# Optimization experiments

Measured on AMD Instinct MI355X. Metric: run time of the kernel, lower is better.

Reference implementation:

```python
import jax, jax.numpy as jnp
import numpy as np

N = 50000
E = 1000000
D_IN = 128
D_HID = 128
D_EMB = 128
D_DEG = 32
NEG_SLOPE = 0.2


def _add_self_loops(src, dst, n):
    loop = jnp.arange(n, dtype=src.dtype)
    return jnp.concatenate([src, loop]), jnp.concatenate([dst, loop])


def gat_conv(x, src, dst, W, a_src, a_dst, b, n):
    """PyG GATConv, heads=1, add_self_loops=True. src/dst already include self loops."""
    h = x @ W                                   # [n, d_out]
    hs = h[src]                                 # [e, d_out] gather (message sources)
    e = jax.nn.leaky_relu(hs @ a_src + h[dst] @ a_dst, NEG_SLOPE)  # [e]
    m = jax.ops.segment_max(e, dst, num_segments=n)
    e = jnp.exp(e - m[dst])
    denom = jax.ops.segment_sum(e, dst, num_segments=n)
    alpha = e / (denom[dst] + 1e-16)
    out = jax.ops.segment_sum(alpha[:, None] * hs, dst, num_segments=n)
    return out + b


def setup_inputs() -> dict:
    key = jax.random.key(0)
    ks = jax.random.split(key, 24)
    p = lambda k, shape: (jax.random.normal(k, shape, dtype=jnp.float32) * 0.05)
    inp = {
        "x_o": jax.random.normal(ks[0], (N, D_IN), dtype=jnp.float32),
        "degree_o": jax.random.normal(ks[1], (N, D_DEG), dtype=jnp.float32),
        "edge_index_o": jax.random.randint(ks[2], (2, E), 0, N, dtype=jnp.int32),
        "edge_index_s": jax.random.randint(ks[3], (2, E), 0, N, dtype=jnp.int32),
        # GAT layer params: o1, o2, s1, s2
        "W_o1": p(ks[4], (D_IN, D_HID)), "a_src_o1": p(ks[5], (D_HID,)), "a_dst_o1": p(ks[6], (D_HID,)), "b_o1": jnp.zeros((D_HID,), jnp.float32),
        "W_o2": p(ks[7], (D_HID, D_EMB)), "a_src_o2": p(ks[8], (D_EMB,)), "a_dst_o2": p(ks[9], (D_EMB,)), "b_o2": jnp.zeros((D_EMB,), jnp.float32),
        "W_s1": p(ks[10], (D_IN, D_HID)), "a_src_s1": p(ks[11], (D_HID,)), "a_dst_s1": p(ks[12], (D_HID,)), "b_s1": jnp.zeros((D_HID,), jnp.float32),
        "W_s2": p(ks[13], (D_HID, D_EMB)), "a_src_s2": p(ks[14], (D_EMB,)), "a_dst_s2": p(ks[15], (D_EMB,)), "b_s2": jnp.zeros((D_EMB,), jnp.float32),
        "W_pred": p(ks[16], (2 * D_EMB + D_DEG, 2)), "b_pred": jnp.zeros((2,), jnp.float32),
    }
    return inp


def reference(x_o, degree_o,
              W_o1, a_src_o1, a_dst_o1, b_o1,
              W_o2, a_src_o2, a_dst_o2, b_o2,
              W_s1, a_src_s1, a_dst_s1, b_s1,
              W_s2, a_src_s2, a_dst_s2, b_s2,
              W_pred, b_pred,
              edge_index_o, edge_index_s):
    n = x_o.shape[0]
    src_o, dst_o = _add_self_loops(edge_index_o[0], edge_index_o[1], n)
    src_s, dst_s = _add_self_loops(edge_index_s[0], edge_index_s[1], n)

    # branch o (original graph); dropout is identity in eval mode
    x1_o = jax.nn.relu(gat_conv(x_o, src_o, dst_o, W_o1, a_src_o1, a_dst_o1, b_o1, n))
    x2_o = gat_conv(x1_o, src_o, dst_o, W_o2, a_src_o2, a_dst_o2, b_o2, n)
    # branch s (second graph)
    x1_s = jax.nn.relu(gat_conv(x_o, src_s, dst_s, W_s1, a_src_s1, a_dst_s1, b_s1, n))
    x2_s = gat_conv(x1_s, src_s, dst_s, W_s2, a_src_s2, a_dst_s2, b_s2, n)

    x2_os = jnp.concatenate([x2_o, x2_s, degree_o], axis=1)   # [n, 2*emb+deg]
    attn = jax.nn.softmax(x2_os @ W_pred + b_pred, axis=1)    # [n, 2]
    pred = attn[:, :1] * x2_o + attn[:, 1:] * x2_s            # [n, emb]
    return pred
```

## Files before the change

kernel.cpp:

```cpp
#include <hip/hip_runtime.h>
#include <hip/hip_fp16.h>
#include <math.h>


#define LRELU(v) ((v) > 0.f ? (v) : 0.2f * (v))

#define BSHIFT 7
#define BSIZE  128
#define MAXB   512
#define CHUNK  4096
#define EPT    16
#define MAXE   4352
#define CAPI   (MAXE + BSIZE)
#define WTSZ   17408

typedef _Float16 half8 __attribute__((ext_vector_type(8)));
typedef float f32x4 __attribute__((ext_vector_type(4)));


__global__ __launch_bounds__(256) void k_bin_scatter(
    const int* __restrict__ src_o, const int* __restrict__ dst_o,
    const int* __restrict__ src_s, const int* __restrict__ dst_s,
    int* bcur_o, int* bcur_s, int* ebin_o, int* ebin_s, int E)
{
    __shared__ int cnt[MAXB];
    __shared__ int gb[MAXB];
    int t = threadIdx.x;
    int base = blockIdx.x * CHUNK;

    for (int g = 0; g < 2; g++) {
        const int* srcp = g ? src_s : src_o;
        const int* dstp = g ? dst_s : dst_o;
        int* bcur = g ? bcur_s : bcur_o;
        int* ebin = g ? ebin_s : ebin_o;
        for (int i = t; i < MAXB; i += 256) cnt[i] = 0;
        __syncthreads();
        int pk[EPT], bk[EPT], rk[EPT];
        #pragma unroll
        for (int j = 0; j < EPT; j++) {
            int e = base + j * 256 + t;
            bk[j] = -1; pk[j] = 0; rk[j] = 0;
            if (e < E) {
                int d = dstp[e];
                int s = srcp[e];
                int bb = d >> BSHIFT;
                bk[j] = bb;
                pk[j] = ((d & (BSIZE - 1)) << 16) | s;
                rk[j] = atomicAdd(&cnt[bb], 1);
            }
        }
        __syncthreads();
        for (int i = t; i < MAXB; i += 256) {
            int c = cnt[i];
            gb[i] = c ? atomicAdd(&bcur[i], c) : 0;
        }
        __syncthreads();
        #pragma unroll
        for (int j = 0; j < EPT; j++) {
            if (bk[j] >= 0) {
                int p = gb[bk[j]] + rk[j];
                if (p < (bk[j] + 1) * MAXE) ebin[p] = pk[j];
            }
        }
        __syncthreads();
    }
}

__global__ __launch_bounds__(256) void k_sort(
    const int* __restrict__ ebin_o, const int* __restrict__ bcur_o,
    int* __restrict__ off_o, int* __restrict__ dend_o, unsigned short* __restrict__ idx_o,
    const int* __restrict__ ebin_s, const int* __restrict__ bcur_s,
    int* __restrict__ off_s, int* __restrict__ dend_s, unsigned short* __restrict__ idx_s,
    int N)
{
    const int* ebin = blockIdx.y ? ebin_s : ebin_o;
    const int* bcur = blockIdx.y ? bcur_s : bcur_o;
    int* off  = blockIdx.y ? off_s  : off_o;
    int* dend = blockIdx.y ? dend_s : dend_o;
    unsigned short* idx = blockIdx.y ? idx_s : idx_o;

    __shared__ int pack[MAXE];
    __shared__ int sorted[MAXE + BSIZE];
    __shared__ int cnt4[4][BSIZE + 1];
    __shared__ int s2[BSIZE + 1];
    __shared__ int noff[BSIZE + 1];

    int b = blockIdx.x;
    int t = threadIdx.x;
    int wave = t >> 6;
    int node0 = b << BSHIFT;
    int nloc = min(BSIZE, N - node0);
    int ebeg = b * MAXE;
    int ne = min(bcur[b] - ebeg, MAXE);
    int ib = b * CAPI;

    for (int i = t; i < ne; i += 256) pack[i] = ebin[ebeg + i];
    for (int i = t; i < 4 * (BSIZE + 1); i += 256) ((int*)cnt4)[i] = 0;
    __syncthreads();
    for (int i = t; i < ne; i += 256) atomicAdd(&cnt4[wave][pack[i] >> 16], 1);
    __syncthreads();
    int c0 = 0, c1 = 0, c2 = 0, c3 = 0, selfc = 0;
    if (t < BSIZE + 1) {
        c0 = cnt4[0][t]; c1 = cnt4[1][t]; c2 = cnt4[2][t]; c3 = cnt4[3][t];
        selfc = (t < nloc) ? 1 : 0;
        s2[t] = c0 + c1 + c2 + c3 + selfc;
    }
    __syncthreads();
    for (int d = 1; d <= BSIZE; d <<= 1) {
        int v = (t < BSIZE + 1 && t >= d) ? s2[t - d] : 0;
        __syncthreads();
        if (t < BSIZE + 1) s2[t] += v;
        __syncthreads();
    }
    if (t < BSIZE + 1) noff[t] = s2[t] - (c0 + c1 + c2 + c3 + selfc);
    __syncthreads();
    if (t < nloc) {
        int base0 = noff[t] + 1;
        cnt4[0][t] = base0;
        cnt4[1][t] = base0 + c0;
        cnt4[2][t] = base0 + c0 + c1;
        cnt4[3][t] = base0 + c0 + c1 + c2;
        sorted[noff[t]] = node0 + t;
        off[node0 + t]  = ib + noff[t];
        dend[node0 + t] = ib + s2[t];
    }
    __syncthreads();
    for (int i = t; i < ne; i += 256) {
        int p = atomicAdd(&cnt4[wave][pack[i] >> 16], 1);
        sorted[p] = pack[i] & 0xffff;
    }
    __syncthreads();
    int tot = ne + nloc;
    for (int i = t; i < tot; i += 256) idx[ib + i] = (unsigned short)sorted[i];
}


__global__ __launch_bounds__(256) void k_prepw(
    const float* __restrict__ W0, const float* __restrict__ W1,
    const float* __restrict__ W2, const float* __restrict__ W3,
    _Float16* __restrict__ WtG, int* bcur_o, int* bcur_s, int nbuck)
{
    int i = blockIdx.x * 256 + threadIdx.x;
    if (i < nbuck) { bcur_o[i] = i * MAXE; bcur_s[i] = i * MAXE; }
    int w = i >> 14;
    int rem = i & 16383;
    int nn = rem >> 7;
    int k = rem & 127;
    const float* W = (w == 0) ? W0 : (w == 1) ? W1 : (w == 2) ? W2 : W3;
    WtG[w * WTSZ + nn * 136 + k] = (_Float16)W[k * 128 + nn];
}


__device__ __forceinline__ void sd_epilogue(
    const f32x4* acc, const float* a_src, const float* a_dst,
    float* Svec, float* Dvec, int m0, int wave, int lane, int m, int q, int n)
{
    float sp[4] = {0.f, 0.f, 0.f, 0.f};
    float dp[4] = {0.f, 0.f, 0.f, 0.f};
    #pragma unroll
    for (int nt = 0; nt < 8; nt++) {
        float asv = a_src[nt * 16 + m];
        float adv = a_dst[nt * 16 + m];
        #pragma unroll
        for (int r = 0; r < 4; r++) {
            sp[r] = fmaf(acc[nt][r], asv, sp[r]);
            dp[r] = fmaf(acc[nt][r], adv, dp[r]);
        }
    }
    #pragma unroll
    for (int msk = 1; msk < 16; msk <<= 1) {
        #pragma unroll
        for (int r = 0; r < 4; r++) {
            sp[r] += __shfl_xor(sp[r], msk);
            dp[r] += __shfl_xor(dp[r], msk);
        }
    }
    if (m == 0) {
        #pragma unroll
        for (int r = 0; r < 4; r++) {
            int row = m0 + wave * 16 + q * 4 + r;
            if (row < n) { Svec[row] = sp[r]; Dvec[row] = dp[r]; }
        }
    }
}

__device__ __forceinline__ void d_to_lds(
    _Float16* As, const f32x4* acc, int wave, int m, int q)
{
    #pragma unroll
    for (int nt = 0; nt < 8; nt++) {
        #pragma unroll
        for (int r = 0; r < 4; r++) {
            As[(wave * 16 + q * 4 + r) * 136 + nt * 16 + m] = (_Float16)acc[nt][r];
        }
    }
}

__device__ __forceinline__ void lds_to_h(
    const _Float16* As, __half* H, int m0, int tid, int n)
{
    for (int i = tid; i < 1024; i += 256) {
        int r = i >> 4;
        int c8 = (i & 15) << 3;
        int row = m0 + r;
        if (row < n)
            *(uint4*)&H[(size_t)row * 128 + c8] = *(const uint4*)&As[r * 136 + c8];
    }
}


__global__ __launch_bounds__(256, 4) void k_gemm1(
    const float* __restrict__ X,
    const _Float16* __restrict__ WtO, const _Float16* __restrict__ WtS,
    const float* __restrict__ asO, const float* __restrict__ adO,
    const float* __restrict__ asS, const float* __restrict__ adS,
    __half* __restrict__ HO, __half* __restrict__ HS,
    float* __restrict__ SO, float* __restrict__ DO,
    float* __restrict__ SS, float* __restrict__ DS, int n)
{
    __shared__ _Float16 As[64 * 136];
    __shared__ _Float16 Wt[128 * 136];
    int tid = threadIdx.x;
    int m0 = blockIdx.x * 64;

    for (int i = tid; i < WTSZ / 8; i += 256)
        ((uint4*)Wt)[i] = ((const uint4*)WtO)[i];
    for (int i = tid; i < 64 * 32; i += 256) {
        int r = i >> 5;
        int c4 = (i & 31) << 2;
        int row = m0 + r; if (row >= n) row = n - 1;
        float4 v = *(const float4*)&X[(size_t)row * 128 + c4];
        _Float16* p = &As[r * 136 + c4];
        p[0] = (_Float16)v.x; p[1] = (_Float16)v.y;
        p[2] = (_Float16)v.z; p[3] = (_Float16)v.w;
    }
    __syncthreads();

    int wave = tid >> 6;
    int lane = tid & 63;
    int m = lane & 15;
    int q = lane >> 4;
    int arow = wave * 16 + m;

    f32x4 accO[8], accS[8];
    #pragma unroll
    for (int nt = 0; nt < 8; nt++) accO[nt] = (f32x4){0.f, 0.f, 0.f, 0.f};
    #pragma unroll
    for (int k0 = 0; k0 < 128; k0 += 32) {
        half8 a = *(half8*)&As[arow * 136 + k0 + q * 8];
        #pragma unroll
        for (int nt = 0; nt < 8; nt++) {
            half8 b = *(half8*)&Wt[(nt * 16 + m) * 136 + k0 + q * 8];
            accO[nt] = __builtin_amdgcn_mfma_f32_16x16x32_f16(a, b, accO[nt], 0, 0, 0);
        }
    }
    sd_epilogue(accO, asO, adO, SO, DO, m0, wave, lane, m, q, n);
    __syncthreads();
    for (int i = tid; i < WTSZ / 8; i += 256)
        ((uint4*)Wt)[i] = ((const uint4*)WtS)[i];
    __syncthreads();
    #pragma unroll
    for (int nt = 0; nt < 8; nt++) accS[nt] = (f32x4){0.f, 0.f, 0.f, 0.f};
    #pragma unroll
    for (int k0 = 0; k0 < 128; k0 += 32) {
        half8 a = *(half8*)&As[arow * 136 + k0 + q * 8];
        #pragma unroll
        for (int nt = 0; nt < 8; nt++) {
            half8 b = *(half8*)&Wt[(nt * 16 + m) * 136 + k0 + q * 8];
            accS[nt] = __builtin_amdgcn_mfma_f32_16x16x32_f16(a, b, accS[nt], 0, 0, 0);
        }
    }
    sd_epilogue(accS, asS, adS, SS, DS, m0, wave, lane, m, q, n);

    __syncthreads();
    d_to_lds(As, accO, wave, m, q);
    __syncthreads();
    lds_to_h(As, HO, m0, tid, n);
    __syncthreads();
    d_to_lds(As, accS, wave, m, q);
    __syncthreads();
    lds_to_h(As, HS, m0, tid, n);
}


__global__ __launch_bounds__(256) void k_gemm2(
    const __half* __restrict__ X0, const __half* __restrict__ X1,
    const _Float16* __restrict__ WtA, const _Float16* __restrict__ WtB,
    const float* __restrict__ as0, const float* __restrict__ ad0,
    const float* __restrict__ as1, const float* __restrict__ ad1,
    __half* __restrict__ H0, __half* __restrict__ H1,
    float* __restrict__ S0, float* __restrict__ D0,
    float* __restrict__ S1, float* __restrict__ D1,
    int n)
{
    int br = blockIdx.y;
    const __half* X = br ? X1 : X0;
    const _Float16* WtGp = br ? WtB : WtA;
    const float* a_src = br ? as1 : as0;
    const float* a_dst = br ? ad1 : ad0;
    __half* H = br ? H1 : H0;
    float* Svec = br ? S1 : S0;
    float* Dvec = br ? D1 : D0;

    __shared__ _Float16 As[64 * 136];
    __shared__ _Float16 Wt[128 * 136];
    int tid = threadIdx.x;
    int m0 = blockIdx.x * 64;

    for (int i = tid; i < WTSZ / 8; i += 256)
        ((uint4*)Wt)[i] = ((const uint4*)WtGp)[i];
    for (int i = tid; i < 64 * 16; i += 256) {
        int r = i >> 4;
        int c8 = (i & 15) << 3;
        int row = m0 + r; if (row >= n) row = n - 1;
        *(uint4*)&As[r * 136 + c8] = *(const uint4*)&X[(size_t)row * 128 + c8];
    }
    __syncthreads();

    int wave = tid >> 6;
    int lane = tid & 63;
    int m = lane & 15;
    int q = lane >> 4;
    int arow = wave * 16 + m;

    f32x4 acc[8];
    #pragma unroll
    for (int nt = 0; nt < 8; nt++) acc[nt] = (f32x4){0.f, 0.f, 0.f, 0.f};
    #pragma unroll
    for (int k0 = 0; k0 < 128; k0 += 32) {
        half8 a = *(half8*)&As[arow * 136 + k0 + q * 8];
        #pragma unroll
        for (int nt = 0; nt < 8; nt++) {
            half8 b = *(half8*)&Wt[(nt * 16 + m) * 136 + k0 + q * 8];
            acc[nt] = __builtin_amdgcn_mfma_f32_16x16x32_f16(a, b, acc[nt], 0, 0, 0);
        }
    }
    sd_epilogue(acc, a_src, a_dst, Svec, Dvec, m0, wave, lane, m, q, n);
    __syncthreads();
    d_to_lds(As, acc, wave, m, q);
    __syncthreads();
    lds_to_h(As, H, m0, tid, n);
}


__device__ __forceinline__ void agg_core(
    const __half* __restrict__ H, const float* __restrict__ Svec, float dn,
    const unsigned short* __restrict__ idx, int beg, int end,
    int lane, int q, int subl, float* acc, float& denom)
{
    #pragma unroll
    for (int j = 0; j < 8; j++) acc[j] = 0.f;
    denom = 0.f;
    for (int base = beg; base < end; base += 64) {
        int cnt = min(64, end - base);
        float w = 0.f;
        int s = 0;
        if (lane < cnt) {
            s = idx[base + lane];
            w = __expf(LRELU(Svec[s] + dn));
        }
        denom += w;
        int cnt16 = (cnt + 15) & ~15;
        for (int kk = 0; kk < cnt16; kk += 16) {
            int k0 = kk + q;
            float w0 = __shfl(w, k0);
            float w1 = __shfl(w, k0 + 4);
            float w2 = __shfl(w, k0 + 8);
            float w3 = __shfl(w, k0 + 12);
            int s0 = __shfl(s, k0);
            int s1 = __shfl(s, k0 + 4);
            int s2 = __shfl(s, k0 + 8);
            int s3 = __shfl(s, k0 + 12);
            uint4 u0 = ((const uint4*)(H + (size_t)s0 * 128))[subl];
            uint4 u1 = ((const uint4*)(H + (size_t)s1 * 128))[subl];
            uint4 u2 = ((const uint4*)(H + (size_t)s2 * 128))[subl];
            uint4 u3 = ((const uint4*)(H + (size_t)s3 * 128))[subl];
            const _Float16* p;
            p = (const _Float16*)&u0;
            #pragma unroll
            for (int j = 0; j < 8; j++) acc[j] = fmaf((float)p[j], w0, acc[j]);
            p = (const _Float16*)&u1;
            #pragma unroll
            for (int j = 0; j < 8; j++) acc[j] = fmaf((float)p[j], w1, acc[j]);
            p = (const _Float16*)&u2;
            #pragma unroll
            for (int j = 0; j < 8; j++) acc[j] = fmaf((float)p[j], w2, acc[j]);
            p = (const _Float16*)&u3;
            #pragma unroll
            for (int j = 0; j < 8; j++) acc[j] = fmaf((float)p[j], w3, acc[j]);
        }
    }
    #pragma unroll
    for (int j = 0; j < 8; j++) {
        acc[j] += __shfl_xor(acc[j], 16);
        acc[j] += __shfl_xor(acc[j], 32);
    }
    #pragma unroll
    for (int o = 32; o; o >>= 1) denom += __shfl_xor(denom, o);
}


__global__ __launch_bounds__(256) void k_agg1(
    const __half* __restrict__ H0, const __half* __restrict__ H1,
    const float* __restrict__ S0, const float* __restrict__ D0,
    const float* __restrict__ S1, const float* __restrict__ D1,
    const int* __restrict__ off0, const int* __restrict__ dend0,
    const unsigned short* __restrict__ idx0,
    const int* __restrict__ off1, const int* __restrict__ dend1,
    const unsigned short* __restrict__ idx1,
    const float* __restrict__ b0, const float* __restrict__ b1,
    __half* __restrict__ out0, __half* __restrict__ out1,
    int n)
{
    int br = blockIdx.y;
    const __half* H = br ? H1 : H0;
    const float* Svec = br ? S1 : S0;
    const float* Dvec = br ? D1 : D0;
    const int* off  = br ? off1  : off0;
    const int* dend = br ? dend1 : dend0;
    const unsigned short* idx = br ? idx1 : idx0;
    const float* bias = br ? b1 : b0;
    __half* out = br ? out1 : out0;

    int wave = threadIdx.x >> 6;
    int lane = threadIdx.x & 63;
    int node = blockIdx.x * 4 + wave;
    if (node >= n) return;

    int q = lane >> 4;
    int subl = lane & 15;
    float acc[8], denom;
    agg_core(H, Svec, Dvec[node], idx, off[node], dend[node],
             lane, q, subl, acc, denom);

    if (q == 0) {
        float inv = 1.f / (denom + 1e-16f);
        int cb = subl << 3;
        half8 hv;
        #pragma unroll
        for (int j = 0; j < 8; j++) {
            float v = fmaxf(acc[j] * inv + bias[cb + j], 0.f);
            hv[j] = (_Float16)v;
        }
        *(half8*)&out[(size_t)node * 128 + cb] = hv;
    }
}


__global__ __launch_bounds__(256) void k_agg_pred(
    const __half* __restrict__ H0, const __half* __restrict__ H1,
    const float* __restrict__ S0, const float* __restrict__ D0,
    const float* __restrict__ S1, const float* __restrict__ D1,
    const int* __restrict__ off0, const int* __restrict__ dend0,
    const unsigned short* __restrict__ idx0,
    const int* __restrict__ off1, const int* __restrict__ dend1,
    const unsigned short* __restrict__ idx1,
    const float* __restrict__ b0, const float* __restrict__ b1,
    const float* __restrict__ deg,
    const float* __restrict__ Wp, const float* __restrict__ bp,
    float* __restrict__ out, int n)
{
    int wave = threadIdx.x >> 6;
    int lane = threadIdx.x & 63;
    int node = blockIdx.x * 4 + wave;
    if (node >= n) return;

    int q = lane >> 4;
    int subl = lane & 15;
    int cb = subl << 3;

    float acc[8], denom;
    float vo[8], vs[8];

    agg_core(H0, S0, D0[node], idx0, off0[node], dend0[node],
             lane, q, subl, acc, denom);
    {
        float inv = 1.f / (denom + 1e-16f);
        #pragma unroll
        for (int j = 0; j < 8; j++) vo[j] = acc[j] * inv + b0[cb + j];
    }
    agg_core(H1, S1, D1[node], idx1, off1[node], dend1[node],
             lane, q, subl, acc, denom);
    {
        float inv = 1.f / (denom + 1e-16f);
        #pragma unroll
        for (int j = 0; j < 8; j++) vs[j] = acc[j] * inv + b1[cb + j];
    }

    if (q == 0) {
        float z0 = 0.f, z1 = 0.f;
        #pragma unroll
        for (int j = 0; j < 8; j++) {
            int c = cb + j;
            z0 = fmaf(vo[j], Wp[c * 2],     z0);
            z1 = fmaf(vo[j], Wp[c * 2 + 1], z1);
            z0 = fmaf(vs[j], Wp[(128 + c) * 2],     z0);
            z1 = fmaf(vs[j], Wp[(128 + c) * 2 + 1], z1);
        }
        float2 dv = *(const float2*)&deg[(size_t)node * 32 + 2 * subl];
        z0 = fmaf(dv.x, Wp[(256 + 2 * subl) * 2],     z0);
        z1 = fmaf(dv.x, Wp[(256 + 2 * subl) * 2 + 1], z1);
        z0 = fmaf(dv.y, Wp[(257 + 2 * subl) * 2],     z0);
        z1 = fmaf(dv.y, Wp[(257 + 2 * subl) * 2 + 1], z1);
        #pragma unroll
        for (int msk = 1; msk < 16; msk <<= 1) {
            z0 += __shfl_xor(z0, msk);
            z1 += __shfl_xor(z1, msk);
        }
        z0 += bp[0];
        z1 += bp[1];
        float mz = fmaxf(z0, z1);
        float e0 = __expf(z0 - mz);
        float e1 = __expf(z1 - mz);
        float a0 = e0 / (e0 + e1);
        float a1 = 1.f - a0;
        float4 r0, r1;
        r0.x = a0 * vo[0] + a1 * vs[0];
        r0.y = a0 * vo[1] + a1 * vs[1];
        r0.z = a0 * vo[2] + a1 * vs[2];
        r0.w = a0 * vo[3] + a1 * vs[3];
        r1.x = a0 * vo[4] + a1 * vs[4];
        r1.y = a0 * vo[5] + a1 * vs[5];
        r1.z = a0 * vo[6] + a1 * vs[6];
        r1.w = a0 * vo[7] + a1 * vs[7];
        *(float4*)&out[(size_t)node * 128 + cb] = r0;
        *(float4*)&out[(size_t)node * 128 + cb + 4] = r1;
    }
}


extern "C" void kernel_launch(void* const* d_in, const int* in_sizes, int n_in,
                              void* d_out, int out_size, void* d_ws, size_t ws_size,
                              hipStream_t stream) {
    const float* x_o    = (const float*)d_in[0];
    const float* degree = (const float*)d_in[1];
    const int*   ei_o   = (const int*)d_in[2];
    const int*   ei_s   = (const int*)d_in[3];
    const float* W_o1 = (const float*)d_in[4];
    const float* asr_o1 = (const float*)d_in[5];
    const float* ads_o1 = (const float*)d_in[6];
    const float* b_o1 = (const float*)d_in[7];
    const float* W_o2 = (const float*)d_in[8];
    const float* asr_o2 = (const float*)d_in[9];
    const float* ads_o2 = (const float*)d_in[10];
    const float* b_o2 = (const float*)d_in[11];
    const float* W_s1 = (const float*)d_in[12];
    const float* asr_s1 = (const float*)d_in[13];
    const float* ads_s1 = (const float*)d_in[14];
    const float* b_s1 = (const float*)d_in[15];
    const float* W_s2 = (const float*)d_in[16];
    const float* asr_s2 = (const float*)d_in[17];
    const float* ads_s2 = (const float*)d_in[18];
    const float* b_s2 = (const float*)d_in[19];
    const float* W_pred = (const float*)d_in[20];
    const float* b_pred = (const float*)d_in[21];
    float* out = (float*)d_out;

    const int N = in_sizes[0] / 128;
    const int E = in_sizes[2] / 2;
    const int NBUCK = (N + BSIZE - 1) >> BSHIFT;

    char* ws = (char*)d_ws;
    size_t o = 0;
    auto alloc = [&](size_t bytes) -> char* {
        char* p = ws + o;
        o += (bytes + 255) & ~(size_t)255;
        return p;
    };
    int* bcur_o = (int*)alloc((size_t)NBUCK * 4);
    int* bcur_s = (int*)alloc((size_t)NBUCK * 4);
    int* off_o  = (int*)alloc((size_t)N * 4);
    int* dend_o = (int*)alloc((size_t)N * 4);
    int* off_s  = (int*)alloc((size_t)N * 4);
    int* dend_s = (int*)alloc((size_t)N * 4);
    unsigned short* idx_o = (unsigned short*)alloc((size_t)NBUCK * CAPI * 2);
    unsigned short* idx_s = (unsigned short*)alloc((size_t)NBUCK * CAPI * 2);
    _Float16* WtG = (_Float16*)alloc((size_t)4 * WTSZ * 2);
    float* Sv_o = (float*)alloc((size_t)N * 4);
    float* Dv_o = (float*)alloc((size_t)N * 4);
    float* Sv_s = (float*)alloc((size_t)N * 4);
    float* Dv_s = (float*)alloc((size_t)N * 4);
    __half* h_o   = (__half*)alloc((size_t)N * 128 * 2);
    __half* h_s   = (__half*)alloc((size_t)N * 128 * 2);
    __half* x1h_o = (__half*)alloc((size_t)N * 128 * 2);
    __half* x1h_s = (__half*)alloc((size_t)N * 128 * 2);
    (void)ws_size;

    int* ebin_o = (int*)h_o;
    int* ebin_s = (int*)h_s;

    dim3 blk(256);
    int gBin  = (E + CHUNK - 1) / CHUNK;
    int gGemm = (N + 63) / 64;
    int gNode = (N + 3) / 4;

    k_prepw<<<256, blk, 0, stream>>>(W_o1, W_o2, W_s1, W_s2, WtG,
                                     bcur_o, bcur_s, NBUCK);
    k_bin_scatter<<<gBin, blk, 0, stream>>>(ei_o, ei_o + E, ei_s, ei_s + E,
                                            bcur_o, bcur_s, ebin_o, ebin_s, E);
    dim3 gSort(NBUCK, 2);
    k_sort<<<gSort, blk, 0, stream>>>(ebin_o, bcur_o, off_o, dend_o, idx_o,
                                      ebin_s, bcur_s, off_s, dend_s, idx_s, N);

    k_gemm1<<<gGemm, blk, 0, stream>>>(
        x_o, WtG, WtG + 2 * WTSZ,
        asr_o1, ads_o1, asr_s1, ads_s1,
        h_o, h_s, Sv_o, Dv_o, Sv_s, Dv_s, N);
    dim3 gA(gNode, 2);
    k_agg1<<<gA, blk, 0, stream>>>(
        h_o, h_s, Sv_o, Dv_o, Sv_s, Dv_s,
        off_o, dend_o, idx_o, off_s, dend_s, idx_s,
        b_o1, b_s1, x1h_o, x1h_s, N);
    dim3 gG(gGemm, 2);
    k_gemm2<<<gG, blk, 0, stream>>>(
        x1h_o, x1h_s, WtG + WTSZ, WtG + 3 * WTSZ,
        asr_o2, ads_o2, asr_s2, ads_s2,
        h_o, h_s, Sv_o, Dv_o, Sv_s, Dv_s, N);
    k_agg_pred<<<gNode, blk, 0, stream>>>(
        h_o, h_s, Sv_o, Dv_o, Sv_s, Dv_s,
        off_o, dend_o, idx_o, off_s, dend_s, idx_s,
        b_o2, b_s2, degree, W_pred, b_pred, out, N);
}
```

Before: 352.9 us.

## Assign one 16-lane group per node in aggregation kernels instead of one wave

The two aggregation kernels now give each destination node a 16-lane group, so a wave handles four nodes instead of one. Each group walks its neighbour list in chunks of 16, broadcasting index and weight by shuffle within the group, and no longer needs the cross-quarter reductions. With about 21 edges per node, this is meant to cut wasted lanes and padding, since the old 64-edge chunks rounded up to 16 left most lanes idle. The trade-offs are less memory-level parallelism per node (one row load per step instead of four) and divergence between groups with different degrees inside a wave.

```diff
diff --git a/kernel.cpp b/kernel.cpp
--- a/kernel.cpp
+++ b/kernel.cpp
@@ -343,60 +343,53 @@
 }
 
 
-__device__ __forceinline__ void agg_core(
+__device__ __forceinline__ void agg_core_g(
     const __half* __restrict__ H, const float* __restrict__ Svec, float dn,
     const unsigned short* __restrict__ idx, int beg, int end,
-    int lane, int q, int subl, float* acc, float& denom)
+    int subl, int grpbase, float* acc, float& denom)
 {
     #pragma unroll
     for (int j = 0; j < 8; j++) acc[j] = 0.f;
     denom = 0.f;
-    for (int base = beg; base < end; base += 64) {
-        int cnt = min(64, end - base);
+    int base = beg;
+    for (; base + 16 <= end; base += 16) {
+        int s = idx[base + subl];
+        float w = __expf(LRELU(Svec[s] + dn));
+        denom += w;
+        #pragma unroll
+        for (int k = 0; k < 16; k++) {
+            int   sk = __shfl(s, grpbase + k);
+            float wk = __shfl(w, grpbase + k);
+            uint4 u = ((const uint4*)(H + (size_t)sk * 128))[subl];
+            const _Float16* p = (const _Float16*)&u;
+            #pragma unroll
+            for (int j = 0; j < 8; j++) acc[j] = fmaf((float)p[j], wk, acc[j]);
+        }
+    }
+    if (base < end) {
+        int cnt = end - base;
+        int s = -1;
         float w = 0.f;
-        int s = 0;
-        if (lane < cnt) {
-            s = idx[base + lane];
+        if (subl < cnt) {
+            s = idx[base + subl];
             w = __expf(LRELU(Svec[s] + dn));
         }
         denom += w;
-        int cnt16 = (cnt + 15) & ~15;
-        for (int kk = 0; kk < cnt16; kk += 16) {
-            int k0 = kk + q;
-            float w0 = __shfl(w, k0);
-            float w1 = __shfl(w, k0 + 4);
-            float w2 = __shfl(w, k0 + 8);
-            float w3 = __shfl(w, k0 + 12);
-            int s0 = __shfl(s, k0);
-            int s1 = __shfl(s, k0 + 4);
-            int s2 = __shfl(s, k0 + 8);
-            int s3 = __shfl(s, k0 + 12);
-            uint4 u0 = ((const uint4*)(H + (size_t)s0 * 128))[subl];
-            uint4 u1 = ((const uint4*)(H + (size_t)s1 * 128))[subl];
-            uint4 u2 = ((const uint4*)(H + (size_t)s2 * 128))[subl];
-            uint4 u3 = ((const uint4*)(H + (size_t)s3 * 128))[subl];
-            const _Float16* p;
-            p = (const _Float16*)&u0;
-            #pragma unroll
-            for (int j = 0; j < 8; j++) acc[j] = fmaf((float)p[j], w0, acc[j]);
-            p = (const _Float16*)&u1;
-            #pragma unroll
-            for (int j = 0; j < 8; j++) acc[j] = fmaf((float)p[j], w1, acc[j]);
-            p = (const _Float16*)&u2;
-            #pragma unroll
-            for (int j = 0; j < 8; j++) acc[j] = fmaf((float)p[j], w2, acc[j]);
-            p = (const _Float16*)&u3;
-            #pragma unroll
-            for (int j = 0; j < 8; j++) acc[j] = fmaf((float)p[j], w3, acc[j]);
-        }
-    }
-    #pragma unroll
-    for (int j = 0; j < 8; j++) {
-        acc[j] += __shfl_xor(acc[j], 16);
-        acc[j] += __shfl_xor(acc[j], 32);
-    }
-    #pragma unroll
-    for (int o = 32; o; o >>= 1) denom += __shfl_xor(denom, o);
+        #pragma unroll
+        for (int k = 0; k < 16; k++) {
+            int   sk = __shfl(s, grpbase + k);
+            float wk = __shfl(w, grpbase + k);
+            if (sk >= 0) {
+                uint4 u = ((const uint4*)(H + (size_t)sk * 128))[subl];
+                const _Float16* p = (const _Float16*)&u;
+                #pragma unroll
+                for (int j = 0; j < 8; j++) acc[j] = fmaf((float)p[j], wk, acc[j]);
+            }
+        }
+    }
+    #pragma unroll
+    for (int msk = 1; msk < 16; msk <<= 1)
+        denom += __shfl_xor(denom, msk);
 }
 
 
@@ -422,28 +415,25 @@
     const float* bias = br ? b1 : b0;
     __half* out = br ? out1 : out0;
 
-    int wave = threadIdx.x >> 6;
-    int lane = threadIdx.x & 63;
-    int node = blockIdx.x * 4 + wave;
+    int tid = threadIdx.x;
+    int node = blockIdx.x * 16 + (tid >> 4);
     if (node >= n) return;
-
-    int q = lane >> 4;
-    int subl = lane & 15;
+    int subl = tid & 15;
+    int grpbase = tid & 48;
+
     float acc[8], denom;
-    agg_core(H, Svec, Dvec[node], idx, off[node], dend[node],
-             lane, q, subl, acc, denom);
-
-    if (q == 0) {
-        float inv = 1.f / (denom + 1e-16f);
-        int cb = subl << 3;
-        half8 hv;
-        #pragma unroll
-        for (int j = 0; j < 8; j++) {
-            float v = fmaxf(acc[j] * inv + bias[cb + j], 0.f);
-            hv[j] = (_Float16)v;
-        }
-        *(half8*)&out[(size_t)node * 128 + cb] = hv;
-    }
+    agg_core_g(H, Svec, Dvec[node], idx, off[node], dend[node],
+               subl, grpbase, acc, denom);
+
+    float inv = 1.f / (denom + 1e-16f);
+    int cb = subl << 3;
+    half8 hv;
+    #pragma unroll
+    for (int j = 0; j < 8; j++) {
+        float v = fmaxf(acc[j] * inv + bias[cb + j], 0.f);
+        hv[j] = (_Float16)v;
+    }
+    *(half8*)&out[(size_t)node * 128 + cb] = hv;
 }
 
 
@@ -460,72 +450,68 @@
     const float* __restrict__ Wp, const float* __restrict__ bp,
     float* __restrict__ out, int n)
 {
-    int wave = threadIdx.x >> 6;
-    int lane = threadIdx.x & 63;
-    int node = blockIdx.x * 4 + wave;
+    int tid = threadIdx.x;
+    int node = blockIdx.x * 16 + (tid >> 4);
     if (node >= n) return;
-
-    int q = lane >> 4;
-    int subl = lane & 15;
+    int subl = tid & 15;
+    int grpbase = tid & 48;
     int cb = subl << 3;
 
     float acc[8], denom;
     float vo[8], vs[8];
 
-    agg_core(H0, S0, D0[node], idx0, off0[node], dend0[node],
-             lane, q, subl, acc, denom);
+    agg_core_g(H0, S0, D0[node], idx0, off0[node], dend0[node],
+               subl, grpbase, acc, denom);
     {
         float inv = 1.f / (denom + 1e-16f);
         #pragma unroll
         for (int j = 0; j < 8; j++) vo[j] = acc[j] * inv + b0[cb + j];
     }
-    agg_core(H1, S1, D1[node], idx1, off1[node], dend1[node],
-             lane, q, subl, acc, denom);
+    agg_core_g(H1, S1, D1[node], idx1, off1[node], dend1[node],
+               subl, grpbase, acc, denom);
     {
         float inv = 1.f / (denom + 1e-16f);
         #pragma unroll
         for (int j = 0; j < 8; j++) vs[j] = acc[j] * inv + b1[cb + j];
     }
 
-    if (q == 0) {
-        float z0 = 0.f, z1 = 0.f;
-        #pragma unroll
-        for (int j = 0; j < 8; j++) {
-            int c = cb + j;
-            z0 = fmaf(vo[j], Wp[c * 2],     z0);
-            z1 = fmaf(vo[j], Wp[c * 2 + 1], z1);
-            z0 = fmaf(vs[j], Wp[(128 + c) * 2],     z0);
-            z1 = fmaf(vs[j], Wp[(128 + c) * 2 + 1], z1);
-        }
-        float2 dv = *(const float2*)&deg[(size_t)node * 32 + 2 * subl];
-        z0 = fmaf(dv.x, Wp[(256 + 2 * subl) * 2],     z0);
-        z1 = fmaf(dv.x, Wp[(256 + 2 * subl) * 2 + 1], z1);
-        z0 = fmaf(dv.y, Wp[(257 + 2 * subl) * 2],     z0);
-        z1 = fmaf(dv.y, Wp[(257 + 2 * subl) * 2 + 1], z1);
-        #pragma unroll
-        for (int msk = 1; msk < 16; msk <<= 1) {
-            z0 += __shfl_xor(z0, msk);
-            z1 += __shfl_xor(z1, msk);
-        }
-        z0 += bp[0];
-        z1 += bp[1];
-        float mz = fmaxf(z0, z1);
-        float e0 = __expf(z0 - mz);
-        float e1 = __expf(z1 - mz);
-        float a0 = e0 / (e0 + e1);
-        float a1 = 1.f - a0;
-        float4 r0, r1;
-        r0.x = a0 * vo[0] + a1 * vs[0];
-        r0.y = a0 * vo[1] + a1 * vs[1];
-        r0.z = a0 * vo[2] + a1 * vs[2];
-        r0.w = a0 * vo[3] + a1 * vs[3];
-        r1.x = a0 * vo[4] + a1 * vs[4];
-        r1.y = a0 * vo[5] + a1 * vs[5];
-        r1.z = a0 * vo[6] + a1 * vs[6];
-        r1.w = a0 * vo[7] + a1 * vs[7];
-        *(float4*)&out[(size_t)node * 128 + cb] = r0;
-        *(float4*)&out[(size_t)node * 128 + cb + 4] = r1;
-    }
+    float z0 = 0.f, z1 = 0.f;
+    #pragma unroll
+    for (int j = 0; j < 8; j++) {
+        int c = cb + j;
+        z0 = fmaf(vo[j], Wp[c * 2],     z0);
+        z1 = fmaf(vo[j], Wp[c * 2 + 1], z1);
+        z0 = fmaf(vs[j], Wp[(128 + c) * 2],     z0);
+        z1 = fmaf(vs[j], Wp[(128 + c) * 2 + 1], z1);
+    }
+    float2 dv = *(const float2*)&deg[(size_t)node * 32 + 2 * subl];
+    z0 = fmaf(dv.x, Wp[(256 + 2 * subl) * 2],     z0);
+    z1 = fmaf(dv.x, Wp[(256 + 2 * subl) * 2 + 1], z1);
+    z0 = fmaf(dv.y, Wp[(257 + 2 * subl) * 2],     z0);
+    z1 = fmaf(dv.y, Wp[(257 + 2 * subl) * 2 + 1], z1);
+    #pragma unroll
+    for (int msk = 1; msk < 16; msk <<= 1) {
+        z0 += __shfl_xor(z0, msk);
+        z1 += __shfl_xor(z1, msk);
+    }
+    z0 += bp[0];
+    z1 += bp[1];
+    float mz = fmaxf(z0, z1);
+    float e0 = __expf(z0 - mz);
+    float e1 = __expf(z1 - mz);
+    float a0 = e0 / (e0 + e1);
+    float a1 = 1.f - a0;
+    float4 r0, r1;
+    r0.x = a0 * vo[0] + a1 * vs[0];
+    r0.y = a0 * vo[1] + a1 * vs[1];
+    r0.z = a0 * vo[2] + a1 * vs[2];
+    r0.w = a0 * vo[3] + a1 * vs[3];
+    r1.x = a0 * vo[4] + a1 * vs[4];
+    r1.y = a0 * vo[5] + a1 * vs[5];
+    r1.z = a0 * vo[6] + a1 * vs[6];
+    r1.w = a0 * vo[7] + a1 * vs[7];
+    *(float4*)&out[(size_t)node * 128 + cb] = r0;
+    *(float4*)&out[(size_t)node * 128 + cb + 4] = r1;
 }
 
 
@@ -592,7 +578,7 @@
     dim3 blk(256);
     int gBin  = (E + CHUNK - 1) / CHUNK;
     int gGemm = (N + 63) / 64;
-    int gNode = (N + 3) / 4;
+    int gN16  = (N + 15) / 16;
 
     k_prepw<<<256, blk, 0, stream>>>(W_o1, W_o2, W_s1, W_s2, WtG,
                                      bcur_o, bcur_s, NBUCK);
@@ -606,7 +592,7 @@
         x_o, WtG, WtG + 2 * WTSZ,
         asr_o1, ads_o1, asr_s1, ads_s1,
         h_o, h_s, Sv_o, Dv_o, Sv_s, Dv_s, N);
-    dim3 gA(gNode, 2);
+    dim3 gA(gN16, 2);
     k_agg1<<<gA, blk, 0, stream>>>(
         h_o, h_s, Sv_o, Dv_o, Sv_s, Dv_s,
         off_o, dend_o, idx_o, off_s, dend_s, idx_s,
@@ -616,7 +602,7 @@
         x1h_o, x1h_s, WtG + WTSZ, WtG + 3 * WTSZ,
         asr_o2, ads_o2, asr_s2, ads_s2,
         h_o, h_s, Sv_o, Dv_o, Sv_s, Dv_s, N);
-    k_agg_pred<<<gNode, blk, 0, stream>>>(
+    k_agg_pred<<<gN16, blk, 0, stream>>>(
         h_o, h_s, Sv_o, Dv_o, Sv_s, Dv_s,
         off_o, dend_o, idx_o, off_s, dend_s, idx_s,
         b_o2, b_s2, degree, W_pred, b_pred, out, N);
```

Result: slower. 386.3 us (+9.5%).

## Merge sort and first GEMM into one heterogeneous launch to overlap them

Applied to the files above, without the earlier changes.

The per-bucket CSR sort and the first-layer GEMM become device functions and are dispatched from one kernel by block index, so sort blocks and GEMM blocks run at the same time. The edge-bin scratch buffers move from h_o/h_s to x1h_o/x1h_s, because the GEMM now writes h while the sort is still reading bins. This removes a launch boundary and lets the two independent stages fill the GPU together. In exchange, both paths share one 52 KB static LDS allocation, and the GEMM loses its occupancy hint of 4 blocks per CU, which may lower its occupancy.

```diff
diff --git a/kernel.cpp b/kernel.cpp
--- a/kernel.cpp
+++ b/kernel.cpp
@@ -66,74 +66,6 @@
     }
 }
 
-__global__ __launch_bounds__(256) void k_sort(
-    const int* __restrict__ ebin_o, const int* __restrict__ bcur_o,
-    int* __restrict__ off_o, int* __restrict__ dend_o, unsigned short* __restrict__ idx_o,
-    const int* __restrict__ ebin_s, const int* __restrict__ bcur_s,
-    int* __restrict__ off_s, int* __restrict__ dend_s, unsigned short* __restrict__ idx_s,
-    int N)
-{
-    const int* ebin = blockIdx.y ? ebin_s : ebin_o;
-    const int* bcur = blockIdx.y ? bcur_s : bcur_o;
-    int* off  = blockIdx.y ? off_s  : off_o;
-    int* dend = blockIdx.y ? dend_s : dend_o;
-    unsigned short* idx = blockIdx.y ? idx_s : idx_o;
-
-    __shared__ int pack[MAXE];
-    __shared__ int sorted[MAXE + BSIZE];
-    __shared__ int cnt4[4][BSIZE + 1];
-    __shared__ int s2[BSIZE + 1];
-    __shared__ int noff[BSIZE + 1];
-
-    int b = blockIdx.x;
-    int t = threadIdx.x;
-    int wave = t >> 6;
-    int node0 = b << BSHIFT;
-    int nloc = min(BSIZE, N - node0);
-    int ebeg = b * MAXE;
-    int ne = min(bcur[b] - ebeg, MAXE);
-    int ib = b * CAPI;
-
-    for (int i = t; i < ne; i += 256) pack[i] = ebin[ebeg + i];
-    for (int i = t; i < 4 * (BSIZE + 1); i += 256) ((int*)cnt4)[i] = 0;
-    __syncthreads();
-    for (int i = t; i < ne; i += 256) atomicAdd(&cnt4[wave][pack[i] >> 16], 1);
-    __syncthreads();
-    int c0 = 0, c1 = 0, c2 = 0, c3 = 0, selfc = 0;
-    if (t < BSIZE + 1) {
-        c0 = cnt4[0][t]; c1 = cnt4[1][t]; c2 = cnt4[2][t]; c3 = cnt4[3][t];
-        selfc = (t < nloc) ? 1 : 0;
-        s2[t] = c0 + c1 + c2 + c3 + selfc;
-    }
-    __syncthreads();
-    for (int d = 1; d <= BSIZE; d <<= 1) {
-        int v = (t < BSIZE + 1 && t >= d) ? s2[t - d] : 0;
-        __syncthreads();
-        if (t < BSIZE + 1) s2[t] += v;
-        __syncthreads();
-    }
-    if (t < BSIZE + 1) noff[t] = s2[t] - (c0 + c1 + c2 + c3 + selfc);
-    __syncthreads();
-    if (t < nloc) {
-        int base0 = noff[t] + 1;
-        cnt4[0][t] = base0;
-        cnt4[1][t] = base0 + c0;
-        cnt4[2][t] = base0 + c0 + c1;
-        cnt4[3][t] = base0 + c0 + c1 + c2;
-        sorted[noff[t]] = node0 + t;
-        off[node0 + t]  = ib + noff[t];
-        dend[node0 + t] = ib + s2[t];
-    }
-    __syncthreads();
-    for (int i = t; i < ne; i += 256) {
-        int p = atomicAdd(&cnt4[wave][pack[i] >> 16], 1);
-        sorted[p] = pack[i] & 0xffff;
-    }
-    __syncthreads();
-    int tot = ne + nloc;
-    for (int i = t; i < tot; i += 256) idx[ib + i] = (unsigned short)sorted[i];
-}
-
 
 __global__ __launch_bounds__(256) void k_prepw(
     const float* __restrict__ W0, const float* __restrict__ W1,
@@ -209,7 +141,73 @@
 }
 
 
-__global__ __launch_bounds__(256, 4) void k_gemm1(
+__device__ __forceinline__ void sort_body(
+    char* SMEM, int b,
+    const int* __restrict__ ebin, const int* __restrict__ bcur,
+    int* __restrict__ off, int* __restrict__ dend,
+    unsigned short* __restrict__ idx, int N)
+{
+    int* pack   = (int*)SMEM;
+    int* sorted = pack + MAXE;
+    int* cnt4   = sorted + MAXE + BSIZE;
+    int* s2     = cnt4 + 4 * (BSIZE + 1);
+    int* noff   = s2 + (BSIZE + 1);
+
+    int t = threadIdx.x;
+    int wave = t >> 6;
+    int node0 = b << BSHIFT;
+    int nloc = min(BSIZE, N - node0);
+    int ebeg = b * MAXE;
+    int ne = min(bcur[b] - ebeg, MAXE);
+    int ib = b * CAPI;
+
+    for (int i = t; i < ne; i += 256) pack[i] = ebin[ebeg + i];
+    for (int i = t; i < 4 * (BSIZE + 1); i += 256) cnt4[i] = 0;
+    __syncthreads();
+    for (int i = t; i < ne; i += 256)
+        atomicAdd(&cnt4[wave * (BSIZE + 1) + (pack[i] >> 16)], 1);
+    __syncthreads();
+    int c0 = 0, c1 = 0, c2 = 0, c3 = 0, selfc = 0;
+    if (t < BSIZE + 1) {
+        c0 = cnt4[0 * (BSIZE + 1) + t];
+        c1 = cnt4[1 * (BSIZE + 1) + t];
+        c2 = cnt4[2 * (BSIZE + 1) + t];
+        c3 = cnt4[3 * (BSIZE + 1) + t];
+        selfc = (t < nloc) ? 1 : 0;
+        s2[t] = c0 + c1 + c2 + c3 + selfc;
+    }
+    __syncthreads();
+    for (int d = 1; d <= BSIZE; d <<= 1) {
+        int v = (t < BSIZE + 1 && t >= d) ? s2[t - d] : 0;
+        __syncthreads();
+        if (t < BSIZE + 1) s2[t] += v;
+        __syncthreads();
+    }
+    if (t < BSIZE + 1) noff[t] = s2[t] - (c0 + c1 + c2 + c3 + selfc);
+    __syncthreads();
+    if (t < nloc) {
+        int base0 = noff[t] + 1;
+        cnt4[0 * (BSIZE + 1) + t] = base0;
+        cnt4[1 * (BSIZE + 1) + t] = base0 + c0;
+        cnt4[2 * (BSIZE + 1) + t] = base0 + c0 + c1;
+        cnt4[3 * (BSIZE + 1) + t] = base0 + c0 + c1 + c2;
+        sorted[noff[t]] = node0 + t;
+        off[node0 + t]  = ib + noff[t];
+        dend[node0 + t] = ib + s2[t];
+    }
+    __syncthreads();
+    for (int i = t; i < ne; i += 256) {
+        int p = atomicAdd(&cnt4[wave * (BSIZE + 1) + (pack[i] >> 16)], 1);
+        sorted[p] = pack[i] & 0xffff;
+    }
+    __syncthreads();
+    int tot = ne + nloc;
+    for (int i = t; i < tot; i += 256) idx[ib + i] = (unsigned short)sorted[i];
+}
+
+
+__device__ __forceinline__ void gemm1_body(
+    char* SMEM, int m0,
     const float* __restrict__ X,
     const _Float16* __restrict__ WtO, const _Float16* __restrict__ WtS,
     const float* __restrict__ asO, const float* __restrict__ adO,
@@ -218,10 +216,9 @@
     float* __restrict__ SO, float* __restrict__ DO,
     float* __restrict__ SS, float* __restrict__ DS, int n)
 {
-    __shared__ _Float16 As[64 * 136];
-    __shared__ _Float16 Wt[128 * 136];
+    _Float16* As = (_Float16*)SMEM;
+    _Float16* Wt = As + 64 * 136;
     int tid = threadIdx.x;
-    int m0 = blockIdx.x * 64;
 
     for (int i = tid; i < WTSZ / 8; i += 256)
         ((uint4*)Wt)[i] = ((const uint4*)WtO)[i];
@@ -280,6 +277,34 @@
     d_to_lds(As, accS, wave, m, q);
     __syncthreads();
     lds_to_h(As, HS, m0, tid, n);
+}
+
+
+__global__ __launch_bounds__(256) void k_sortgemm1(
+    const int* __restrict__ ebin_o, const int* __restrict__ bcur_o,
+    int* __restrict__ off_o, int* __restrict__ dend_o, unsigned short* __restrict__ idx_o,
+    const int* __restrict__ ebin_s, const int* __restrict__ bcur_s,
+    int* __restrict__ off_s, int* __restrict__ dend_s, unsigned short* __restrict__ idx_s,
+    const float* __restrict__ X,
+    const _Float16* __restrict__ WtO, const _Float16* __restrict__ WtS,
+    const float* __restrict__ asO, const float* __restrict__ adO,
+    const float* __restrict__ asS, const float* __restrict__ adS,
+    __half* __restrict__ HO, __half* __restrict__ HS,
+    float* __restrict__ SO, float* __restrict__ DO,
+    float* __restrict__ SS, float* __restrict__ DS,
+    int N, int nbuck)
+{
+    __shared__ __align__(16) char SMEM[52224];
+    int bid = blockIdx.x;
+    if (bid < 2 * nbuck) {
+        if (bid < nbuck)
+            sort_body(SMEM, bid, ebin_o, bcur_o, off_o, dend_o, idx_o, N);
+        else
+            sort_body(SMEM, bid - nbuck, ebin_s, bcur_s, off_s, dend_s, idx_s, N);
+    } else {
+        gemm1_body(SMEM, (bid - 2 * nbuck) * 64, X, WtO, WtS,
+                   asO, adO, asS, adS, HO, HS, SO, DO, SS, DS, N);
+    }
 }
 
 
@@ -586,8 +611,8 @@
     __half* x1h_s = (__half*)alloc((size_t)N * 128 * 2);
     (void)ws_size;
 
-    int* ebin_o = (int*)h_o;
-    int* ebin_s = (int*)h_s;
+    int* ebin_o = (int*)x1h_o;
+    int* ebin_s = (int*)x1h_s;
 
     dim3 blk(256);
     int gBin  = (E + CHUNK - 1) / CHUNK;
@@ -598,14 +623,12 @@
                                      bcur_o, bcur_s, NBUCK);
     k_bin_scatter<<<gBin, blk, 0, stream>>>(ei_o, ei_o + E, ei_s, ei_s + E,
                                             bcur_o, bcur_s, ebin_o, ebin_s, E);
-    dim3 gSort(NBUCK, 2);
-    k_sort<<<gSort, blk, 0, stream>>>(ebin_o, bcur_o, off_o, dend_o, idx_o,
-                                      ebin_s, bcur_s, off_s, dend_s, idx_s, N);
-
-    k_gemm1<<<gGemm, blk, 0, stream>>>(
+    k_sortgemm1<<<2 * NBUCK + gGemm, blk, 0, stream>>>(
+        ebin_o, bcur_o, off_o, dend_o, idx_o,
+        ebin_s, bcur_s, off_s, dend_s, idx_s,
         x_o, WtG, WtG + 2 * WTSZ,
         asr_o1, ads_o1, asr_s1, ads_s1,
-        h_o, h_s, Sv_o, Dv_o, Sv_s, Dv_s, N);
+        h_o, h_s, Sv_o, Dv_o, Sv_s, Dv_s, N, NBUCK);
     dim3 gA(gNode, 2);
     k_agg1<<<gA, blk, 0, stream>>>(
         h_o, h_s, Sv_o, Dv_o, Sv_s, Dv_s,
```

Measured after the change: 351.9 us. No clear change (-0.3%).
